# Performance work log

Hardware: AMD Instinct MI355X
Metric: run time of the kernel (lower is better)

The kernel has to match this reference:

```python
import jax, jax.numpy as jnp
import numpy as np

C = 1024      # channels
H = 16        # num_heads
D = C // H    # head_dim = 64
K = 64        # max_kernel_size
MAX_FREQ = 16.0
MIN_FREQ = 1.0
HALF_S = 16   # from max_samples=32, ndim=1 -> offsets -16..16 (S=33)
MAX_RECEPTIVE = HALF_S * MAX_FREQ  # 256.0
EPS = 1e-6


def rmsnorm(x, w):
    # LlamaRMSNorm: fp32 accumulation, scale by learned gamma
    xf = x.astype(jnp.float32)
    var = jnp.mean(xf * xf, axis=-1, keepdims=True)
    return (w * (xf * jax.lax.rsqrt(var + EPS))).astype(x.dtype)


def setup_inputs() -> dict:
    key = jax.random.key(0)
    ks = jax.random.split(key, 7)
    B, L = 2, 2048
    return {
        "x": jax.random.normal(ks[0], (B, L, C), jnp.float32),
        "w_wave": jax.random.normal(ks[1], (2 * H, C), jnp.float32) * 0.02,
        "b_wave": jax.random.normal(ks[2], (2 * H,), jnp.float32) * 0.02,
        "g_wave": jnp.ones((2 * H,), jnp.float32),
        "w_kern": jax.random.normal(ks[3], (H * K, C), jnp.float32) * 0.02,
        "b_kern": jnp.zeros((H * K,), jnp.float32),
        "g_kern": jnp.ones((H * K,), jnp.float32),
        "w_exp": jax.random.normal(ks[4], (1, C), jnp.float32) * 0.02,
        "b_exp": jnp.zeros((1,), jnp.float32),
        "g_exp": jnp.ones((1,), jnp.float32),
        "w_out": jax.random.normal(ks[5], (C, C), jnp.float32) * 0.02,
    }


def reference(x, w_wave, b_wave, g_wave, w_kern, b_kern, g_kern,
              w_exp, b_exp, g_exp, w_out):
    B, L, _ = x.shape
    dt = x.dtype
    offsets = jnp.arange(-HALF_S, HALF_S + 1, dtype=dt)  # (S,) S=33

    # wave params -> per-token, per-head freq & phase
    wave = jax.nn.silu(rmsnorm(x @ w_wave.T + b_wave, g_wave)).reshape(B, L, 2, H)
    freq = jax.nn.sigmoid(wave[:, :, 0]) * (MAX_FREQ - MIN_FREQ) + MIN_FREQ  # (B,L,H)
    phase = jnp.tanh(wave[:, :, 1]) * MAX_FREQ                               # (B,L,H)

    # learned sample positions with bilinear (linear in 1D) interpolation
    centers = jnp.arange(L, dtype=dt)
    pos = centers[None, :, None, None] + offsets * freq[..., None] + phase[..., None]  # (B,L,H,S)
    valid = ((pos >= 0) & (pos < L)).astype(dt)
    pc = jnp.clip(pos, 0.0, L - 1.001)
    fl = jnp.clip(jnp.floor(pc).astype(jnp.int32), 0, L - 1)
    cl = jnp.minimum(fl + 1, L - 1)
    frac = pc - fl.astype(dt)
    rel = offsets * freq[..., None]  # (B,L,H,S)

    # per-token kernel projection + interpolation to sample positions
    kernel_max = jax.nn.silu(rmsnorm(x @ w_kern.T + b_kern, g_kern)).reshape(B, L, H, K)
    exponent = jax.nn.sigmoid(rmsnorm(x @ w_exp.T + b_exp, g_exp)) * 3.5 + 0.5  # (B,L,1)
    power = 1.0 / jnp.power(1.0 + jnp.abs(rel) / L, exponent[..., None])        # (B,L,H,S)

    idx_f = jnp.clip(jnp.abs(rel) / MAX_RECEPTIVE, 0.0, 1.0) * (K - 1)
    i0 = jnp.clip(idx_f.astype(jnp.int32), 0, K - 2)
    i1 = i0 + 1
    wc = idx_f - i0.astype(dt)
    wf = 1.0 - wc
    k0 = jnp.take_along_axis(kernel_max, i0, axis=-1)
    k1 = jnp.take_along_axis(kernel_max, i1, axis=-1)
    kern = (k0 * wf + k1 * wc) * power * valid  # (B,L,H,S)

    # gather values at floor/ceil positions and interpolate
    xh = x.reshape(B, L, H, D)
    bidx = jnp.arange(B)[:, None, None, None]
    hidx = jnp.arange(H)[None, None, :, None]
    vf = xh[bidx, fl, hidx]  # (B,L,H,S,D)
    vc = xh[bidx, cl, hidx]
    val = vf * (1.0 - frac[..., None]) + vc * frac[..., None]

    hidden = jnp.einsum('blhs,blhsd->blhd', kern, val).reshape(B, L, C)
    return jax.nn.silu(hidden @ w_out.T)
```

## Files before the change

kernel.cpp:

```cpp
#include <hip/hip_runtime.h>
#include <hip/hip_bf16.h>
#include <math.h>

#define B_ 2
#define L_ 2048
#define C_ 1024
#define H_ 16
#define D_ 64
#define K_ 64
#define S_ 33
#define M_ (B_*L_)

typedef _Float16 half8 __attribute__((ext_vector_type(8)));
typedef float f32x4 __attribute__((ext_vector_type(4)));

__device__ __forceinline__ float sigmoidf_(float v) { return 1.f / (1.f + __expf(-v)); }

__global__ __launch_bounds__(256) void conv_w(
    const float* __restrict__ w_kern, const float* __restrict__ w_out,
    _Float16* __restrict__ wkh, _Float16* __restrict__ woh)
{
  int i = blockIdx.x * 256 + threadIdx.x;
  const float* src; _Float16* dst; int j;
  if (i < 131072) { src = w_kern; dst = wkh; j = i; }
  else            { src = w_out;  dst = woh; j = i - 131072; }
  float4 a = ((const float4*)src)[j * 2];
  float4 b = ((const float4*)src)[j * 2 + 1];
  half8 v;
  v[0] = (_Float16)a.x; v[1] = (_Float16)a.y; v[2] = (_Float16)a.z; v[3] = (_Float16)a.w;
  v[4] = (_Float16)b.x; v[5] = (_Float16)b.y; v[6] = (_Float16)b.z; v[7] = (_Float16)b.w;
  ((half8*)dst)[j] = v;
}

__global__ __launch_bounds__(256) void prep(
    const float* __restrict__ x,
    const float* __restrict__ w_wave, const float* __restrict__ b_wave,
    const float* __restrict__ g_wave,
    const float* __restrict__ w_exp, const float* __restrict__ b_exp,
    const float* __restrict__ g_exp,
    _Float16* __restrict__ xh,
    float* __restrict__ freq, float* __restrict__ phase, float* __restrict__ expn)
{
  __shared__ float xs[4 * C_];
  __shared__ float dots[4][S_];
  int bid = blockIdx.x;
  int tid = threadIdx.x;
  int lane = tid & 63, wv = tid >> 6;
  int m0 = bid * 4;

#pragma unroll
  for (int q = 0; q < 4; q++) {
    int idx = tid + q * 256;
    ((float4*)xs)[idx] = ((const float4*)(x + (size_t)m0 * C_))[idx];
  }
  __syncthreads();

#pragma unroll
  for (int q = 0; q < 2; q++) {
    int i8 = tid + q * 256;
    float4 a = ((const float4*)xs)[i8 * 2];
    float4 b = ((const float4*)xs)[i8 * 2 + 1];
    half8 v;
    v[0] = (_Float16)a.x; v[1] = (_Float16)a.y; v[2] = (_Float16)a.z; v[3] = (_Float16)a.w;
    v[4] = (_Float16)b.x; v[5] = (_Float16)b.y; v[6] = (_Float16)b.z; v[7] = (_Float16)b.w;
    ((half8*)(xh + (size_t)m0 * C_))[i8] = v;
  }

  const float* xrow = xs + wv * C_;
  for (int n = 0; n < 33; n++) {
    const float* wr = (n < 32) ? (w_wave + n * C_) : w_exp;
    float s = 0.f;
#pragma unroll
    for (int q = 0; q < 4; q++) {
      int k4 = lane + q * 64;
      float4 xv = ((const float4*)xrow)[k4];
      float4 wv4 = ((const float4*)wr)[k4];
      s += xv.x * wv4.x + xv.y * wv4.y + xv.z * wv4.z + xv.w * wv4.w;
    }
    for (int o = 32; o; o >>= 1) s += __shfl_xor(s, o);
    if (lane == 0) dots[wv][n] = s + ((n < 32) ? b_wave[n] : b_exp[0]);
  }
  __syncthreads();

  int m = m0 + wv;
  float v = (lane < 32) ? dots[wv][lane] : 0.f;
  float ss = v * v;
  for (int o = 32; o; o >>= 1) ss += __shfl_xor(ss, o);
  float scale = rsqrtf(ss * (1.f / 32.f) + 1e-6f);
  if (lane < 32) {
    float nv = dots[wv][lane] * scale * g_wave[lane];
    float sv = nv * sigmoidf_(nv);
    if (lane < 16) freq[m * H_ + lane] = sigmoidf_(sv) * 15.f + 1.f;
    else           phase[m * H_ + lane - 16] = tanhf(sv) * 16.f;
  }
  if (lane == 0) {
    float y = dots[wv][32];
    float nv = y * rsqrtf(y * y + 1e-6f) * g_exp[0];
    expn[m] = sigmoidf_(nv) * 3.5f + 0.5f;
  }
}

template<int SILU, int OUTH>
__global__ __launch_bounds__(256) void gemm_h(
    const _Float16* __restrict__ A, const _Float16* __restrict__ Bw,
    void* __restrict__ Co_v, int M, int N, int Kd)
{
  __shared__ __align__(16) _Float16 As[64 * 32];
  __shared__ __align__(16) _Float16 Bs[128 * 32];
  int tid = threadIdx.x;
  int m0 = blockIdx.y * 64, n0 = blockIdx.x * 128;
  int lane = tid & 63;
  int w = tid >> 6;

  f32x4 acc[4][2];
#pragma unroll
  for (int i = 0; i < 4; i++)
#pragma unroll
    for (int j = 0; j < 2; j++)
      acc[i][j] = (f32x4){0.f, 0.f, 0.f, 0.f};

  for (int k0 = 0; k0 < Kd; k0 += 32) {
    {
      int row = tid >> 2, seg = tid & 3;
      int sseg = seg ^ (row & 3);
      const _Float16* ga = A + (size_t)(m0 + row) * Kd + k0 + sseg * 8;
      __builtin_amdgcn_global_load_lds(
          (const __attribute__((address_space(1))) unsigned int*)ga,
          (__attribute__((address_space(3))) unsigned int*)&As[tid * 8], 16, 0, 0);
    }
#pragma unroll
    for (int q = 0; q < 2; q++) {
      int idx = tid + q * 256;
      int row = idx >> 2, seg = idx & 3;
      int sseg = seg ^ (row & 3);
      const _Float16* gb = Bw + (size_t)(n0 + row) * Kd + k0 + sseg * 8;
      __builtin_amdgcn_global_load_lds(
          (const __attribute__((address_space(1))) unsigned int*)gb,
          (__attribute__((address_space(3))) unsigned int*)&Bs[idx * 8], 16, 0, 0);
    }
    __syncthreads();

    half8 aF[4], bF[2];
#pragma unroll
    for (int i = 0; i < 4; i++) {
      int ar = i * 16 + (lane & 15);
      int ac = (lane >> 4) ^ (ar & 3);
      aF[i] = *(const half8*)&As[ar * 32 + ac * 8];
    }
#pragma unroll
    for (int j = 0; j < 2; j++) {
      int br = w * 32 + j * 16 + (lane & 15);
      int bc = (lane >> 4) ^ (br & 3);
      bF[j] = *(const half8*)&Bs[br * 32 + bc * 8];
    }
#pragma unroll
    for (int i = 0; i < 4; i++)
#pragma unroll
      for (int j = 0; j < 2; j++)
        acc[i][j] = __builtin_amdgcn_mfma_f32_16x16x32_f16(aF[i], bF[j], acc[i][j], 0, 0, 0);
    __syncthreads();
  }

#pragma unroll
  for (int i = 0; i < 4; i++)
#pragma unroll
    for (int j = 0; j < 2; j++) {
      int col = n0 + w * 32 + j * 16 + (lane & 15);
#pragma unroll
      for (int r = 0; r < 4; r++) {
        int row = m0 + i * 16 + (lane >> 4) * 4 + r;
        float t = acc[i][j][r];
        if (SILU) t = t * sigmoidf_(t);
        if (OUTH) ((_Float16*)Co_v)[(size_t)row * N + col] = (_Float16)t;
        else      ((float*)Co_v)[(size_t)row * N + col] = t;
      }
    }
}

__global__ __launch_bounds__(256) void sampler(
    const _Float16* __restrict__ xh, const _Float16* __restrict__ ykr,
    const float* __restrict__ b_kern, const float* __restrict__ g_kern,
    const float* __restrict__ freq, const float* __restrict__ phase,
    const float* __restrict__ expn, _Float16* __restrict__ hidden)
{
  __shared__ float km[2][C_];
  __shared__ float kw[2][H_][S_];
  __shared__ float fr[2][H_][S_];
  __shared__ int   fli[2][H_][S_];
  __shared__ float red2[2][2];
  int bid = blockIdx.x;
  int pair = ((bid & 7) << 8) + (bid >> 3);
  int tid = threadIdx.x;
  int sub = tid >> 7, t = tid & 127;
  int m = pair * 2 + sub;
  int b = m >> 11, l = m & (L_ - 1);
  int lane = tid & 63;

  float yv[8];
  {
    half8 hv = *(const half8*)(ykr + (size_t)m * C_ + t * 8);
    float ss = 0.f;
#pragma unroll
    for (int j = 0; j < 8; j++) {
      yv[j] = (float)hv[j] + b_kern[t * 8 + j];
      ss += yv[j] * yv[j];
    }
    for (int o = 32; o; o >>= 1) ss += __shfl_xor(ss, o);
    if (lane == 0) red2[sub][t >> 6] = ss;
  }
  __syncthreads();
  {
    float scale = rsqrtf((red2[sub][0] + red2[sub][1]) * (1.f / 1024.f) + 1e-6f);
#pragma unroll
    for (int j = 0; j < 8; j++) {
      float nv = yv[j] * scale * g_kern[t * 8 + j];
      km[sub][t * 8 + j] = nv * sigmoidf_(nv);
    }
  }
  __syncthreads();

  float e = expn[m];
  for (int i = t; i < H_ * S_; i += 128) {
    int h = i / S_, s = i - h * S_;
    float f  = freq[m * H_ + h];
    float ph = phase[m * H_ + h];
    float rel = (float)(s - 16) * f;
    float posv = (float)l + rel + ph;
    float kern = 0.f, frac = 0.f;
    int fl = 0;
    if (posv >= 0.f && posv < 2048.f) {
      float pc = fminf(posv, 2046.999f);
      fl = (int)pc;
      frac = pc - (float)fl;
      float ar = fabsf(rel);
      float idx_f = fminf(ar * (1.f / 256.f), 1.f) * 63.f;
      int i0 = (int)idx_f; if (i0 > 62) i0 = 62;
      float wc = idx_f - (float)i0;
      float k0 = km[sub][(h << 6) + i0];
      float k1 = km[sub][(h << 6) + i0 + 1];
      float powv = __expf(-e * __logf(1.f + ar * (1.f / 2048.f)));
      kern = (k0 * (1.f - wc) + k1 * wc) * powv;
    }
    kw[sub][h][s] = kern; fr[sub][h][s] = frac; fli[sub][h][s] = fl;
  }
  __syncthreads();

  int h = t >> 3, d8 = (t & 7) << 3;
  const _Float16* xb = xh + (size_t)b * L_ * C_ + (h << 6) + d8;
  float acc[8] = {0.f, 0.f, 0.f, 0.f, 0.f, 0.f, 0.f, 0.f};
#pragma unroll 4
  for (int s = 0; s < S_; s++) {
    float kern = kw[sub][h][s];
    float frac = fr[sub][h][s];
    int fl = fli[sub][h][s];
    const _Float16* pf = xb + (size_t)fl * C_;
    half8 vf = *(const half8*)pf;
    half8 vc = *(const half8*)(pf + C_);
    float wf = kern * (1.f - frac), wcf = kern * frac;
#pragma unroll
    for (int j = 0; j < 8; j++)
      acc[j] += wf * (float)vf[j] + wcf * (float)vc[j];
  }
  half8 o8;
#pragma unroll
  for (int j = 0; j < 8; j++) o8[j] = (_Float16)acc[j];
  *(half8*)(hidden + (size_t)m * C_ + (h << 6) + d8) = o8;
}

extern "C" void kernel_launch(void* const* d_in, const int* in_sizes, int n_in,
                              void* d_out, int out_size, void* d_ws, size_t ws_size,
                              hipStream_t stream) {
  const float* x      = (const float*)d_in[0];
  const float* w_wave = (const float*)d_in[1];
  const float* b_wave = (const float*)d_in[2];
  const float* g_wave = (const float*)d_in[3];
  const float* w_kern = (const float*)d_in[4];
  const float* b_kern = (const float*)d_in[5];
  const float* g_kern = (const float*)d_in[6];
  const float* w_exp  = (const float*)d_in[7];
  const float* b_exp  = (const float*)d_in[8];
  const float* g_exp  = (const float*)d_in[9];
  const float* w_out  = (const float*)d_in[10];
  float* out = (float*)d_out;

  char* ws = (char*)d_ws;
  _Float16* ykh    = (_Float16*)ws;
  _Float16* xhp    = (_Float16*)(ws + (size_t) 8 * 1024 * 1024);
  _Float16* hidden = (_Float16*)(ws + (size_t)16 * 1024 * 1024);
  _Float16* wkh    = (_Float16*)(ws + (size_t)24 * 1024 * 1024);
  _Float16* woh    = (_Float16*)(ws + (size_t)26 * 1024 * 1024);
  float*    freqb  = (float*)(ws + (size_t)28 * 1024 * 1024);
  float*    phaseb = freqb + (size_t)M_ * H_;
  float*    expnb  = phaseb + (size_t)M_ * H_;

  conv_w<<<1024, 256, 0, stream>>>(w_kern, w_out, wkh, woh);
  prep<<<M_ / 4, 256, 0, stream>>>(x, w_wave, b_wave, g_wave, w_exp, b_exp, g_exp,
                                   xhp, freqb, phaseb, expnb);
  dim3 gg(C_ / 128, M_ / 64);
  gemm_h<0,1><<<gg, 256, 0, stream>>>(xhp, wkh, ykh, M_, C_, C_);
  sampler<<<M_ / 2, 256, 0, stream>>>(xhp, ykh, b_kern, g_kern,
                                      freqb, phaseb, expnb, hidden);
  gemm_h<1,0><<<gg, 256, 0, stream>>>(hidden, woh, out, M_, C_, C_);
}
```

Before: 190.5 us.

## Use 128x128 tiles with split-K=2 GEMMs and separate reduction epilogue

```diff
diff --git a/kernel.cpp b/kernel.cpp
--- a/kernel.cpp
+++ b/kernel.cpp
@@ -100,85 +100,96 @@
   }
 }
 
-template<int SILU, int OUTH>
-__global__ __launch_bounds__(256) void gemm_h(
+__global__ __launch_bounds__(256) void gemm_sk(
     const _Float16* __restrict__ A, const _Float16* __restrict__ Bw,
-    void* __restrict__ Co_v, int M, int N, int Kd)
-{
-  __shared__ __align__(16) _Float16 As[64 * 32];
+    _Float16* __restrict__ Cp, int M, int N, int Kd)
+{
+  __shared__ __align__(16) _Float16 As[128 * 32];
   __shared__ __align__(16) _Float16 Bs[128 * 32];
   int tid = threadIdx.x;
-  int m0 = blockIdx.y * 64, n0 = blockIdx.x * 128;
+  int m0 = blockIdx.y * 128, n0 = blockIdx.x * 128;
+  int z = blockIdx.z;
+  int kbase = z * (Kd >> 1);
   int lane = tid & 63;
-  int w = tid >> 6;
-
-  f32x4 acc[4][2];
+  int wid = tid >> 6, wm = wid >> 1, wn = wid & 1;
+
+  f32x4 acc[4][4];
 #pragma unroll
   for (int i = 0; i < 4; i++)
 #pragma unroll
-    for (int j = 0; j < 2; j++)
+    for (int j = 0; j < 4; j++)
       acc[i][j] = (f32x4){0.f, 0.f, 0.f, 0.f};
 
-  for (int k0 = 0; k0 < Kd; k0 += 32) {
-    {
-      int row = tid >> 2, seg = tid & 3;
-      int sseg = seg ^ (row & 3);
-      const _Float16* ga = A + (size_t)(m0 + row) * Kd + k0 + sseg * 8;
-      __builtin_amdgcn_global_load_lds(
-          (const __attribute__((address_space(1))) unsigned int*)ga,
-          (__attribute__((address_space(3))) unsigned int*)&As[tid * 8], 16, 0, 0);
-    }
+  for (int k0 = 0; k0 < (Kd >> 1); k0 += 32) {
 #pragma unroll
     for (int q = 0; q < 2; q++) {
       int idx = tid + q * 256;
       int row = idx >> 2, seg = idx & 3;
       int sseg = seg ^ (row & 3);
-      const _Float16* gb = Bw + (size_t)(n0 + row) * Kd + k0 + sseg * 8;
+      const _Float16* ga = A  + (size_t)(m0 + row) * Kd + kbase + k0 + sseg * 8;
+      const _Float16* gb = Bw + (size_t)(n0 + row) * Kd + kbase + k0 + sseg * 8;
+      __builtin_amdgcn_global_load_lds(
+          (const __attribute__((address_space(1))) unsigned int*)ga,
+          (__attribute__((address_space(3))) unsigned int*)&As[idx * 8], 16, 0, 0);
       __builtin_amdgcn_global_load_lds(
           (const __attribute__((address_space(1))) unsigned int*)gb,
           (__attribute__((address_space(3))) unsigned int*)&Bs[idx * 8], 16, 0, 0);
     }
     __syncthreads();
 
-    half8 aF[4], bF[2];
+    half8 aF[4], bF[4];
 #pragma unroll
     for (int i = 0; i < 4; i++) {
-      int ar = i * 16 + (lane & 15);
+      int ar = wm * 64 + i * 16 + (lane & 15);
       int ac = (lane >> 4) ^ (ar & 3);
       aF[i] = *(const half8*)&As[ar * 32 + ac * 8];
     }
 #pragma unroll
-    for (int j = 0; j < 2; j++) {
-      int br = w * 32 + j * 16 + (lane & 15);
+    for (int j = 0; j < 4; j++) {
+      int br = wn * 64 + j * 16 + (lane & 15);
       int bc = (lane >> 4) ^ (br & 3);
       bF[j] = *(const half8*)&Bs[br * 32 + bc * 8];
     }
 #pragma unroll
     for (int i = 0; i < 4; i++)
 #pragma unroll
-      for (int j = 0; j < 2; j++)
+      for (int j = 0; j < 4; j++)
         acc[i][j] = __builtin_amdgcn_mfma_f32_16x16x32_f16(aF[i], bF[j], acc[i][j], 0, 0, 0);
     __syncthreads();
   }
 
+  _Float16* Cz = Cp + (size_t)z * M * N;
 #pragma unroll
   for (int i = 0; i < 4; i++)
 #pragma unroll
-    for (int j = 0; j < 2; j++) {
-      int col = n0 + w * 32 + j * 16 + (lane & 15);
+    for (int j = 0; j < 4; j++) {
+      int col = n0 + wn * 64 + j * 16 + (lane & 15);
 #pragma unroll
       for (int r = 0; r < 4; r++) {
-        int row = m0 + i * 16 + (lane >> 4) * 4 + r;
-        float t = acc[i][j][r];
-        if (SILU) t = t * sigmoidf_(t);
-        if (OUTH) ((_Float16*)Co_v)[(size_t)row * N + col] = (_Float16)t;
-        else      ((float*)Co_v)[(size_t)row * N + col] = t;
+        int row = m0 + wm * 64 + i * 16 + (lane >> 4) * 4 + r;
+        Cz[(size_t)row * N + col] = (_Float16)acc[i][j][r];
       }
     }
 }
 
+__global__ __launch_bounds__(256) void epi(
+    const _Float16* __restrict__ hp, float* __restrict__ out)
+{
+  int i = blockIdx.x * 256 + threadIdx.x;
+  half8 a = ((const half8*)hp)[i];
+  half8 b = ((const half8*)(hp + (size_t)M_ * C_))[i];
+  float o[8];
+#pragma unroll
+  for (int j = 0; j < 8; j++) {
+    float t = (float)a[j] + (float)b[j];
+    o[j] = t * sigmoidf_(t);
+  }
+  ((float4*)out)[i * 2]     = make_float4(o[0], o[1], o[2], o[3]);
+  ((float4*)out)[i * 2 + 1] = make_float4(o[4], o[5], o[6], o[7]);
+}
+
 __global__ __launch_bounds__(256) void sampler(
-    const _Float16* __restrict__ xh, const _Float16* __restrict__ ykr,
+    const _Float16* __restrict__ xh, const _Float16* __restrict__ ykp,
     const float* __restrict__ b_kern, const float* __restrict__ g_kern,
     const float* __restrict__ freq, const float* __restrict__ phase,
     const float* __restrict__ expn, _Float16* __restrict__ hidden)
@@ -198,11 +209,12 @@
 
   float yv[8];
   {
-    half8 hv = *(const half8*)(ykr + (size_t)m * C_ + t * 8);
+    half8 h0 = *(const half8*)(ykp + (size_t)m * C_ + t * 8);
+    half8 h1 = *(const half8*)(ykp + (size_t)M_ * C_ + (size_t)m * C_ + t * 8);
     float ss = 0.f;
 #pragma unroll
     for (int j = 0; j < 8; j++) {
-      yv[j] = (float)hv[j] + b_kern[t * 8 + j];
+      yv[j] = (float)h0[j] + (float)h1[j] + b_kern[t * 8 + j];
       ss += yv[j] * yv[j];
     }
     for (int o = 32; o; o >>= 1) ss += __shfl_xor(ss, o);
@@ -284,21 +296,23 @@
   float* out = (float*)d_out;
 
   char* ws = (char*)d_ws;
-  _Float16* ykh    = (_Float16*)ws;
-  _Float16* xhp    = (_Float16*)(ws + (size_t) 8 * 1024 * 1024);
-  _Float16* hidden = (_Float16*)(ws + (size_t)16 * 1024 * 1024);
-  _Float16* wkh    = (_Float16*)(ws + (size_t)24 * 1024 * 1024);
-  _Float16* woh    = (_Float16*)(ws + (size_t)26 * 1024 * 1024);
-  float*    freqb  = (float*)(ws + (size_t)28 * 1024 * 1024);
+  _Float16* xhp    = (_Float16*)ws;
+  _Float16* hidden = (_Float16*)(ws + (size_t) 8 * 1024 * 1024);
+  _Float16* ykp    = (_Float16*)(ws + (size_t)16 * 1024 * 1024);
+  _Float16* hp     = (_Float16*)(ws + (size_t)32 * 1024 * 1024);
+  _Float16* wkh    = (_Float16*)(ws + (size_t)48 * 1024 * 1024);
+  _Float16* woh    = (_Float16*)(ws + (size_t)50 * 1024 * 1024);
+  float*    freqb  = (float*)(ws + (size_t)52 * 1024 * 1024);
   float*    phaseb = freqb + (size_t)M_ * H_;
   float*    expnb  = phaseb + (size_t)M_ * H_;
 
   conv_w<<<1024, 256, 0, stream>>>(w_kern, w_out, wkh, woh);
   prep<<<M_ / 4, 256, 0, stream>>>(x, w_wave, b_wave, g_wave, w_exp, b_exp, g_exp,
                                    xhp, freqb, phaseb, expnb);
-  dim3 gg(C_ / 128, M_ / 64);
-  gemm_h<0,1><<<gg, 256, 0, stream>>>(xhp, wkh, ykh, M_, C_, C_);
-  sampler<<<M_ / 2, 256, 0, stream>>>(xhp, ykh, b_kern, g_kern,
+  dim3 gg(C_ / 128, M_ / 128, 2);
+  gemm_sk<<<gg, 256, 0, stream>>>(xhp, wkh, ykp, M_, C_, C_);
+  sampler<<<M_ / 2, 256, 0, stream>>>(xhp, ykp, b_kern, g_kern,
                                       freqb, phaseb, expnb, hidden);
-  gemm_h<1,0><<<gg, 256, 0, stream>>>(hidden, woh, out, M_, C_, C_);
-}
+  gemm_sk<<<gg, 256, 0, stream>>>(hidden, woh, hp, M_, C_, C_);
+  epi<<<(M_ * C_) / 2048, 256, 0, stream>>>(hp, out);
+}
```

Measured after the change: 187.0 us. No clear change (-1.8%).
